# Kernel optimization log

Hardware: AMD Instinct MI355X
Metric: run time of the kernel (lower is better)

Reference implementation:

```python
import jax, jax.numpy as jnp
import numpy as np

D_MODEL = 1024
N_HEAD = 16
HEAD_DIM = D_MODEL // N_HEAD


def setup_inputs() -> dict:
    key = jax.random.key(0)
    ks = jax.random.split(key, 5)
    B, T = 2, 2048
    s = 1.0 / np.sqrt(D_MODEL)
    return {
        "x": jax.random.normal(ks[0], (B, T, D_MODEL), dtype=jnp.float32),
        "w_qkv": jax.random.normal(ks[1], (D_MODEL, 3 * D_MODEL), dtype=jnp.float32) * s,
        "b_qkv": jnp.zeros((3 * D_MODEL,), dtype=jnp.float32),
        "w_proj": jax.random.normal(ks[2], (D_MODEL, D_MODEL), dtype=jnp.float32) * s,
        "b_proj": jnp.zeros((D_MODEL,), dtype=jnp.float32),
    }


def reference(x, w_qkv, b_qkv, w_proj, b_proj):
    B, T, C = x.shape
    H, Dh = N_HEAD, HEAD_DIM
    scale = Dh ** -0.5
    qkv = x @ w_qkv + b_qkv                      # [B,T,3C]
    q, k, v = jnp.split(qkv, 3, axis=2)
    # [B,T,C] -> [B,H,T,Dh]
    q = q.reshape(B, T, H, Dh).transpose(0, 2, 1, 3)
    k = k.reshape(B, T, H, Dh).transpose(0, 2, 1, 3)
    v = v.reshape(B, T, H, Dh).transpose(0, 2, 1, 3)
    att = jnp.einsum("bhqd,bhkd->bhqk", q, k) * scale  # [B,H,T,T]
    causal = jnp.tril(jnp.ones((T, T), dtype=bool))
    att = jnp.where(causal, att, -jnp.inf)
    att = jax.nn.softmax(att, axis=-1)
    out = jnp.einsum("bhqk,bhkd->bhqd", att, v)  # [B,H,T,Dh]
    out = out.transpose(0, 2, 1, 3).reshape(B, T, C)
    return out @ w_proj + b_proj
```

## Files before the change

kernel.cpp:

```cpp
#include <hip/hip_runtime.h>
#include <hip/hip_bf16.h>

#define B_ 2
#define T_ 2048
#define C_ 1024
#define H_ 16
#define DH_ 64

typedef __attribute__((ext_vector_type(8))) short bf16x8;
typedef __attribute__((ext_vector_type(4))) float f32x4;
typedef __attribute__((ext_vector_type(4))) unsigned int u32x4;

#define DEVI static __device__ __forceinline__

DEVI unsigned short f2bf(float f) {
  unsigned int u = __float_as_uint(f);
  u = (u + 0x7fffu + ((u >> 16) & 1u)) >> 16;
  return (unsigned short)u;
}

DEVI f32x4 mfma16(bf16x8 a, bf16x8 b, f32x4 c) {
  return __builtin_amdgcn_mfma_f32_16x16x32_bf16(a, b, c, 0, 0, 0);
}

DEVI void gload_lds16(const unsigned short* g, unsigned short* l) {
  __builtin_amdgcn_global_load_lds(
      (const __attribute__((address_space(1))) unsigned int*)g,
      (__attribute__((address_space(3))) unsigned int*)l, 16, 0, 0);
}

DEVI unsigned int cvtpk_bf16(float lo, float hi) {
  unsigned int r;
  asm("v_cvt_pk_bf16_f32 %0, %1, %2" : "=v"(r) : "v"(lo), "v"(hi));
  return r;
}

DEVI int kperm(int kv) {
  return (kv & 3) | (((kv >> 3) & 1) << 2) | (((kv >> 5) & 1) << 3) |
         (((kv >> 2) & 1) << 4) | (((kv >> 4) & 1) << 5);
}

__global__ __launch_bounds__(256) void prep_kernel(
    const float* __restrict__ x, const float* __restrict__ w_qkv,
    const float* __restrict__ w_proj, unsigned short* __restrict__ xb,
    unsigned short* __restrict__ wqkvT, unsigned short* __restrict__ wprojT) {
  __shared__ float tile[32][33];
  int b = blockIdx.x, tid = threadIdx.x;
  if (b < 4096) {
    int i = b * 256 + tid;
    float4 v = reinterpret_cast<const float4*>(x)[i];
    ushort4 o;
    o.x = f2bf(v.x); o.y = f2bf(v.y); o.z = f2bf(v.z); o.w = f2bf(v.w);
    reinterpret_cast<ushort4*>(xb)[i] = o;
  } else {
    const float* in;
    unsigned short* out;
    int R, C, bb;
    if (b < 7168) { bb = b - 4096; in = w_qkv; out = wqkvT; R = 1024; C = 3072; }
    else          { bb = b - 7168; in = w_proj; out = wprojT; R = 1024; C = 1024; }
    int nbx = C >> 5;
    int c0 = (bb % nbx) * 32, r0 = (bb / nbx) * 32;
    int tx = tid & 31, ty = tid >> 5;
#pragma unroll
    for (int j = 0; j < 32; j += 8)
      tile[ty + j][tx] = in[(size_t)(r0 + ty + j) * C + c0 + tx];
    __syncthreads();
#pragma unroll
    for (int j = 0; j < 32; j += 8)
      out[(size_t)(c0 + ty + j) * R + r0 + tx] = f2bf(tile[tx][ty + j]);
  }
}

__global__ __launch_bounds__(256, 2) void gemm192_qkv(
    const unsigned short* __restrict__ A, const unsigned short* __restrict__ Bt,
    const float* __restrict__ bias,
    unsigned short* __restrict__ qbuf, unsigned short* __restrict__ kbuf,
    unsigned short* __restrict__ vtbuf) {
  __shared__ __attribute__((aligned(16))) unsigned short As[2][128 * 64];
  __shared__ __attribute__((aligned(16))) unsigned short Bs[2][192 * 64];
  const int Kd = 1024;
  int tid = threadIdx.x;
  int lane = tid & 63, w = tid >> 6;
  int wn = w;
  int lrow = lane & 15, lgrp = lane >> 4;

  int g = blockIdx.x;
  int gs = (g & 7) * 64 + (g >> 3);
  int by = gs >> 4, bx = gs & 15;
  int bm = by * 128, bn = bx * 192;
  const unsigned short* Ab = A + (size_t)bm * Kd;
  const unsigned short* Bb = Bt + (size_t)bn * Kd;

  int sL[2], scl[2];
#pragma unroll
  for (int it = 0; it < 2; ++it) {
    int c = tid + it * 256;
    int L = c >> 3, s = c & 7, v = s ^ (L & 7);
    sL[it] = L;
    scl[it] = (v >> 2) * 32 + (v & 3) * 8;
  }

  auto stgA = [&](int t, int h) {
    unsigned short* dst = As[t & 1] + h * 4096;
    int k0 = t << 6;
#pragma unroll
    for (int it = 0; it < 2; ++it)
      gload_lds16(Ab + (size_t)(h * 64 + sL[it]) * Kd + k0 + scl[it],
                  dst + (tid + it * 256) * 8);
  };
  auto stgB3 = [&](int t, int th) {
    unsigned short* dst = Bs[t & 1] + th * 4096;
    int k0 = t << 6;
#pragma unroll
    for (int it = 0; it < 2; ++it)
      gload_lds16(Bb + (size_t)(th * 64 + sL[it]) * Kd + k0 + scl[it],
                  dst + (tid + it * 256) * 8);
  };

  auto lda = [&](const unsigned short* buf, int mi, int kk) -> bf16x8 {
    int row = mi * 16 + lrow;
    int s = ((kk << 2) | lgrp) ^ (row & 7);
    return *reinterpret_cast<const bf16x8*>((const char*)buf + row * 128 + s * 16);
  };
  auto ldb = [&](const unsigned short* buf, int ni, int kk) -> bf16x8 {
    int row = wn * 48 + ni * 16 + lrow;
    int s = ((kk << 2) | lgrp) ^ (row & 7);
    return *reinterpret_cast<const bf16x8*>((const char*)buf + row * 128 + s * 16);
  };

  f32x4 acc[8][3] = {};
  bf16x8 bfr[3][2], af[2][2];

#define PHASE_TAIL                                          \
  __builtin_amdgcn_s_barrier();                             \
  asm volatile("s_waitcnt lgkmcnt(0)" ::: "memory");        \
  __builtin_amdgcn_sched_barrier(0);                        \
  __builtin_amdgcn_s_setprio(1);

#define MFMA_TRI(base)                                      \
  _Pragma("unroll") for (int ii = 0; ii < 2; ++ii)          \
  _Pragma("unroll") for (int ni = 0; ni < 3; ++ni) {        \
    acc[(base) + ii][ni] = mfma16(af[ii][0], bfr[ni][0], acc[(base) + ii][ni]); \
    acc[(base) + ii][ni] = mfma16(af[ii][1], bfr[ni][1], acc[(base) + ii][ni]); \
  }

#define PHASE_END                                           \
  __builtin_amdgcn_s_setprio(0);                            \
  __builtin_amdgcn_s_barrier();

  stgA(0, 0); stgA(0, 1);
  stgB3(0, 0); stgB3(0, 1); stgB3(0, 2);
  stgB3(1, 0); stgB3(1, 1); stgB3(1, 2);
  asm volatile("s_waitcnt vmcnt(6)" ::: "memory");
  __builtin_amdgcn_s_barrier();

#pragma unroll 1
  for (int j = 0; j < 8; ++j) {
    const bool nl = (j < 7);
    const int t1 = 2 * j + 1, t2 = 2 * j + 2, t3 = 2 * j + 3;

#pragma unroll
    for (int ni = 0; ni < 3; ++ni) { bfr[ni][0] = ldb(Bs[0], ni, 0); bfr[ni][1] = ldb(Bs[0], ni, 1); }
    af[0][0] = lda(As[0], 0, 0); af[0][1] = lda(As[0], 0, 1);
    af[1][0] = lda(As[0], 1, 0); af[1][1] = lda(As[0], 1, 1);
    stgA(t1, 0);
    PHASE_TAIL; MFMA_TRI(0); PHASE_END;

    af[0][0] = lda(As[0], 2, 0); af[0][1] = lda(As[0], 2, 1);
    af[1][0] = lda(As[0], 3, 0); af[1][1] = lda(As[0], 3, 1);
    stgA(t1, 1);
    if (nl) stgB3(t2, 0);
    PHASE_TAIL; MFMA_TRI(2); PHASE_END;

    af[0][0] = lda(As[0], 4, 0); af[0][1] = lda(As[0], 4, 1);
    af[1][0] = lda(As[0], 5, 0); af[1][1] = lda(As[0], 5, 1);
    if (nl) stgB3(t2, 1);
    PHASE_TAIL; MFMA_TRI(4); PHASE_END;

    af[0][0] = lda(As[0], 6, 0); af[0][1] = lda(As[0], 6, 1);
    af[1][0] = lda(As[0], 7, 0); af[1][1] = lda(As[0], 7, 1);
    if (nl) stgB3(t2, 2);
    PHASE_TAIL; MFMA_TRI(6);
    __builtin_amdgcn_s_setprio(0);
    if (nl) { asm volatile("s_waitcnt vmcnt(6)" ::: "memory"); }
    else    { asm volatile("s_waitcnt vmcnt(0)" ::: "memory"); }
    __builtin_amdgcn_s_barrier();

#pragma unroll
    for (int ni = 0; ni < 3; ++ni) { bfr[ni][0] = ldb(Bs[1], ni, 0); bfr[ni][1] = ldb(Bs[1], ni, 1); }
    af[0][0] = lda(As[1], 0, 0); af[0][1] = lda(As[1], 0, 1);
    af[1][0] = lda(As[1], 1, 0); af[1][1] = lda(As[1], 1, 1);
    if (nl) stgA(t2, 0);
    PHASE_TAIL; MFMA_TRI(0); PHASE_END;

    af[0][0] = lda(As[1], 2, 0); af[0][1] = lda(As[1], 2, 1);
    af[1][0] = lda(As[1], 3, 0); af[1][1] = lda(As[1], 3, 1);
    if (nl) { stgA(t2, 1); stgB3(t3, 0); }
    PHASE_TAIL; MFMA_TRI(2); PHASE_END;

    af[0][0] = lda(As[1], 4, 0); af[0][1] = lda(As[1], 4, 1);
    af[1][0] = lda(As[1], 5, 0); af[1][1] = lda(As[1], 5, 1);
    if (nl) stgB3(t3, 1);
    PHASE_TAIL; MFMA_TRI(4); PHASE_END;

    af[0][0] = lda(As[1], 6, 0); af[0][1] = lda(As[1], 6, 1);
    af[1][0] = lda(As[1], 7, 0); af[1][1] = lda(As[1], 7, 1);
    if (nl) stgB3(t3, 2);
    PHASE_TAIL; MFMA_TRI(6);
    __builtin_amdgcn_s_setprio(0);
    if (nl) { asm volatile("s_waitcnt vmcnt(6)" ::: "memory"); }
    __builtin_amdgcn_s_barrier();
  }
#undef PHASE_TAIL
#undef MFMA_TRI
#undef PHASE_END

  int c0 = bn + wn * 48;
#pragma unroll
  for (int ni = 0; ni < 3; ++ni) {
    int col = c0 + ni * 16 + lrow;
    float bv = bias[col];
    int which = col >> 10, cc = col & 1023;
    int h = cc >> 6, d = cc & 63;
#pragma unroll
    for (int mi = 0; mi < 8; ++mi) {
      int rowb = bm + mi * 16 + lgrp * 4;
      int b = rowb >> 11, tt = rowb & 2047;
      if (which == 2) {
        ushort4 pk;
        pk.x = f2bf(acc[mi][ni][0] + bv);
        pk.y = f2bf(acc[mi][ni][1] + bv);
        pk.z = f2bf(acc[mi][ni][2] + bv);
        pk.w = f2bf(acc[mi][ni][3] + bv);
        *reinterpret_cast<ushort4*>(vtbuf + ((size_t)((b * 16 + h) * 64 + d)) * T_ + tt) = pk;
      } else {
        unsigned short* dst = (which == 0) ? qbuf : kbuf;
        size_t base = ((size_t)(b * 16 + h) * T_ + tt) * DH_ + d;
#pragma unroll
        for (int r = 0; r < 4; ++r)
          dst[base + (size_t)r * DH_] = f2bf(acc[mi][ni][r] + bv);
      }
    }
  }
}

__global__ __launch_bounds__(256) void gemm_proj(
    const unsigned short* __restrict__ A, const unsigned short* __restrict__ Bt,
    const float* __restrict__ bias, float* __restrict__ outp,
    int Ndim, int Kdim) {
  __shared__ __attribute__((aligned(16))) unsigned short As[128 * 32];
  __shared__ __attribute__((aligned(16))) unsigned short Bs[128 * 32];
  int tid = threadIdx.x;
  int lane = tid & 63, w = tid >> 6;
  int wm = w >> 1, wn = w & 1;
  int lrow = lane & 15, lgrp = lane >> 4;
  int bm = blockIdx.y * 128, bn = blockIdx.x * 128;
  const unsigned short* Ab = A + (size_t)bm * Kdim;
  const unsigned short* Bb = Bt + (size_t)bn * Kdim;

  f32x4 acc[4][4] = {};
  int nk = Kdim >> 5;
  for (int kt = 0; kt < nk; ++kt) {
    int k0 = kt << 5;
    __syncthreads();
#pragma unroll
    for (int it = 0; it < 2; ++it) {
      int c = tid + it * 256;
      int row = c >> 2, kc = (c & 3) << 3;
      gload_lds16(Ab + (size_t)row * Kdim + k0 + kc, As + (size_t)c * 8);
      gload_lds16(Bb + (size_t)row * Kdim + k0 + kc, Bs + (size_t)c * 8);
    }
    __syncthreads();
    bf16x8 af[4], bfr[4];
#pragma unroll
    for (int mi = 0; mi < 4; ++mi)
      af[mi] = *reinterpret_cast<const bf16x8*>(As + (size_t)(wm * 64 + mi * 16 + lrow) * 32 + lgrp * 8);
#pragma unroll
    for (int ni = 0; ni < 4; ++ni)
      bfr[ni] = *reinterpret_cast<const bf16x8*>(Bs + (size_t)(wn * 64 + ni * 16 + lrow) * 32 + lgrp * 8);
#pragma unroll
    for (int mi = 0; mi < 4; ++mi)
#pragma unroll
      for (int ni = 0; ni < 4; ++ni)
        acc[mi][ni] = mfma16(af[mi], bfr[ni], acc[mi][ni]);
  }

  int r0 = bm + wm * 64, c0 = bn + wn * 64;
#pragma unroll
  for (int ni = 0; ni < 4; ++ni) {
    int col = c0 + ni * 16 + lrow;
    float bv = bias[col];
#pragma unroll
    for (int mi = 0; mi < 4; ++mi) {
      int rowb = r0 + mi * 16 + lgrp * 4;
#pragma unroll
      for (int r = 0; r < 4; ++r)
        outp[(size_t)(rowb + r) * Ndim + col] = acc[mi][ni][r] + bv;
    }
  }
}

__global__ __launch_bounds__(256, 4) void attn_kernel(
    const unsigned short* __restrict__ qbuf,
    const unsigned short* __restrict__ kbuf,
    const unsigned short* __restrict__ vtbuf,
    unsigned short* __restrict__ attno) {
  __shared__ __attribute__((aligned(16))) unsigned short Ks[64 * 64];
  __shared__ __attribute__((aligned(16))) unsigned short Vts[64 * 64];

  int tid = threadIdx.x;
  int lane = tid & 63, w = tid >> 6;
  int lrow = lane & 15, lgrp = lane >> 4;

  int g = blockIdx.x;
  int s = g >> 8;
  int p = (g >> 3) & 7;
  int bh = (g & 7) | (((g >> 6) & 3) << 3);
  int qb = (s == 0) ? p : (s == 1) ? (31 - p) : (s == 2) ? (8 + p) : (23 - p);
  int wq0 = qb * 64 + w * 16;
  int nkb = qb + 1;

  const unsigned short* Qb = qbuf + (size_t)bh * T_ * DH_;
  const unsigned short* Kb = kbuf + (size_t)bh * T_ * DH_;
  const unsigned short* Vb = vtbuf + (size_t)bh * DH_ * T_;

  int srow0 = tid >> 3, scol = tid & 7;
  int srow1 = srow0 + 32;
  int pk0 = kperm(srow0), pk1 = kperm(srow1);
  int soffK0 = pk0 * 128 + ((scol * 16) ^ ((pk0 & 7) << 4));
  int soffK1 = pk1 * 128 + ((scol * 16) ^ ((pk1 & 7) << 4));
  int soffV0 = srow0 * 128 + ((scol * 16) ^ ((srow0 & 7) << 4));
  int soffV1 = srow1 * 128 + ((scol * 16) ^ ((srow1 & 7) << 4));

  const float SC = 0.125f * 1.44269504f;
  int kvbase = ((lgrp & 1) << 3) | ((lgrp >> 1) << 5);
  const int koff[4] = {0, 4, 16, 20};

  bf16x8 qf[2];
#pragma unroll
  for (int ks = 0; ks < 2; ++ks)
    qf[ks] = *reinterpret_cast<const bf16x8*>(
        Qb + (size_t)(wq0 + lrow) * DH_ + ks * 32 + lgrp * 8);

  f32x4 o[4] = {};
  float l_run = 0.f;

  bf16x8 sk0, sk1, sv0, sv1;
  auto stage_load = [&](int kb) {
    sk0 = *reinterpret_cast<const bf16x8*>(Kb + (size_t)(kb * 64 + srow0) * DH_ + scol * 8);
    sk1 = *reinterpret_cast<const bf16x8*>(Kb + (size_t)(kb * 64 + srow1) * DH_ + scol * 8);
    sv0 = *reinterpret_cast<const bf16x8*>(Vb + (size_t)srow0 * T_ + kb * 64 + scol * 8);
    sv1 = *reinterpret_cast<const bf16x8*>(Vb + (size_t)srow1 * T_ + kb * 64 + scol * 8);
  };
  auto stage_write = [&]() {
    *reinterpret_cast<bf16x8*>((char*)Ks + soffK0) = sk0;
    *reinterpret_cast<bf16x8*>((char*)Ks + soffK1) = sk1;
    *reinterpret_cast<bf16x8*>((char*)Vts + soffV0) = sv0;
    *reinterpret_cast<bf16x8*>((char*)Vts + soffV1) = sv1;
  };

  stage_load(0);
#pragma unroll 1
  for (int kb = 0; kb < nkb; ++kb) {
    if (kb > 0) __syncthreads();
    stage_write();
    __syncthreads();
    if (kb + 1 < nkb) stage_load(kb + 1);

    f32x4 sreg[4] = {};
#pragma unroll
    for (int ks = 0; ks < 2; ++ks) {
      bf16x8 kf[4];
#pragma unroll
      for (int ni = 0; ni < 4; ++ni) {
        int kr = ni * 16 + lrow;
        int off = kr * 128 + (((ks * 32 + lgrp * 8) * 2) ^ ((kr & 7) << 4));
        kf[ni] = *reinterpret_cast<const bf16x8*>((const char*)Ks + off);
      }
      __builtin_amdgcn_s_setprio(1);
#pragma unroll
      for (int ni = 0; ni < 4; ++ni)
        sreg[ni] = mfma16(kf[ni], qf[ks], sreg[ni]);
      __builtin_amdgcn_s_setprio(0);
    }

    if (kb == qb) {
      int q = wq0 + lrow;
#pragma unroll
      for (int ni = 0; ni < 4; ++ni) {
        int kvb = kb * 64 + kvbase + koff[ni];
#pragma unroll
        for (int r = 0; r < 4; ++r)
          if (kvb + r > q) sreg[ni][r] = -1e30f;
      }
    }

    f32x4 e[4];
#pragma unroll
    for (int ni = 0; ni < 4; ++ni)
#pragma unroll
      for (int r = 0; r < 4; ++r)
        e[ni][r] = __builtin_amdgcn_exp2f(sreg[ni][r] * SC);

    f32x4 ts = (e[0] + e[1]) + (e[2] + e[3]);
    l_run += (ts[0] + ts[1]) + (ts[2] + ts[3]);

    unsigned int Aw[4], Bw[4];
    Aw[0] = cvtpk_bf16(e[0][0], e[0][1]); Aw[1] = cvtpk_bf16(e[0][2], e[0][3]);
    Aw[2] = cvtpk_bf16(e[1][0], e[1][1]); Aw[3] = cvtpk_bf16(e[1][2], e[1][3]);
    Bw[0] = cvtpk_bf16(e[2][0], e[2][1]); Bw[1] = cvtpk_bf16(e[2][2], e[2][3]);
    Bw[2] = cvtpk_bf16(e[3][0], e[3][1]); Bw[3] = cvtpk_bf16(e[3][2], e[3][3]);
    u32x4 p0v, p1v;
#pragma unroll
    for (int ww = 0; ww < 4; ++ww) {
      auto sw = __builtin_amdgcn_permlane32_swap(Aw[ww], Bw[ww], false, false);
      p0v[ww] = sw[0];
      p1v[ww] = sw[1];
    }
    bf16x8 pa[2];
    pa[0] = __builtin_bit_cast(bf16x8, p0v);
    pa[1] = __builtin_bit_cast(bf16x8, p1v);

#pragma unroll
    for (int ks = 0; ks < 2; ++ks) {
      bf16x8 vf[4];
#pragma unroll
      for (int di = 0; di < 4; ++di) {
        int vr = di * 16 + lrow;
        int off = vr * 128 + (((ks * 32 + lgrp * 8) * 2) ^ ((vr & 7) << 4));
        vf[di] = *reinterpret_cast<const bf16x8*>((const char*)Vts + off);
      }
      __builtin_amdgcn_s_setprio(1);
#pragma unroll
      for (int di = 0; di < 4; ++di)
        o[di] = mfma16(pa[ks], vf[di], o[di]);
      __builtin_amdgcn_s_setprio(0);
    }
  }

  float rs = l_run;
  rs += __shfl_xor(rs, 16);
  rs += __shfl_xor(rs, 32);
  float linv = 1.0f / rs;

  int b = bh >> 4, h = bh & 15;
  float lr[4];
#pragma unroll
  for (int r = 0; r < 4; ++r) lr[r] = __shfl(linv, lgrp * 4 + r);
#pragma unroll
  for (int r = 0; r < 4; ++r) {
    int q = wq0 + lgrp * 4 + r;
    size_t base = ((size_t)(b * T_ + q)) * C_ + h * 64 + lrow;
#pragma unroll
    for (int di = 0; di < 4; ++di)
      attno[base + (size_t)di * 16] = f2bf(o[di][r] * lr[r]);
  }
}

extern "C" void kernel_launch(void* const* d_in, const int* in_sizes, int n_in,
                              void* d_out, int out_size, void* d_ws, size_t ws_size,
                              hipStream_t stream) {
  const float* x      = (const float*)d_in[0];
  const float* w_qkv  = (const float*)d_in[1];
  const float* b_qkv  = (const float*)d_in[2];
  const float* w_proj = (const float*)d_in[3];
  const float* b_proj = (const float*)d_in[4];

  char* ws = (char*)d_ws;
  unsigned short* xb     = (unsigned short*)(ws + 0);
  unsigned short* wqkvT  = (unsigned short*)(ws + 8388608);
  unsigned short* wprojT = (unsigned short*)(ws + 14680064);
  unsigned short* qbuf   = (unsigned short*)(ws + 16777216);
  unsigned short* kbuf   = (unsigned short*)(ws + 25165824);
  unsigned short* vtbuf  = (unsigned short*)(ws + 33554432);
  unsigned short* attno  = (unsigned short*)(ws + 41943040);

  prep_kernel<<<8192, 256, 0, stream>>>(x, w_qkv, w_proj, xb, wqkvT, wprojT);
  gemm192_qkv<<<dim3(512), 256, 0, stream>>>(xb, wqkvT, b_qkv, qbuf, kbuf, vtbuf);
  attn_kernel<<<dim3(1024), 256, 0, stream>>>(qbuf, kbuf, vtbuf, attno);
  gemm_proj<<<dim3(8, 32), 256, 0, stream>>>(attno, wprojT, b_proj, (float*)d_out,
                                             1024, 1024);
}
```

Measured before the change: 98.20 us.

## Rewrite projection GEMM with double-buffered swizzled LDS pipeline and block remap

Replaces the simple single-buffered projection GEMM with a double-buffered, BK=64 pipeline. Global-to-LDS loads for later k-tiles are interleaved between MFMA phases, LDS rows use an XOR swizzle to avoid bank conflicts, wave priority is raised around the MFMA sections, and a 1D grid is remapped for L2 locality. The aim is to hide global load latency and LDS conflicts in the output projection. The cost is larger LDS use, hard-coded dimensions and more complex barrier/waitcnt logic.

```diff
diff --git a/kernel.cpp b/kernel.cpp
--- a/kernel.cpp
+++ b/kernel.cpp
@@ -244,58 +244,156 @@
   }
 }
 
-__global__ __launch_bounds__(256) void gemm_proj(
+__global__ __launch_bounds__(256, 2) void gemm_proj(
     const unsigned short* __restrict__ A, const unsigned short* __restrict__ Bt,
-    const float* __restrict__ bias, float* __restrict__ outp,
-    int Ndim, int Kdim) {
-  __shared__ __attribute__((aligned(16))) unsigned short As[128 * 32];
-  __shared__ __attribute__((aligned(16))) unsigned short Bs[128 * 32];
+    const float* __restrict__ bias, float* __restrict__ outp) {
+  __shared__ __attribute__((aligned(16))) unsigned short As[2][128 * 64];
+  __shared__ __attribute__((aligned(16))) unsigned short Bs[2][128 * 64];
+  const int Kd = 1024, Nd = 1024;
   int tid = threadIdx.x;
   int lane = tid & 63, w = tid >> 6;
-  int wm = w >> 1, wn = w & 1;
+  int wn = w;
   int lrow = lane & 15, lgrp = lane >> 4;
-  int bm = blockIdx.y * 128, bn = blockIdx.x * 128;
-  const unsigned short* Ab = A + (size_t)bm * Kdim;
-  const unsigned short* Bb = Bt + (size_t)bn * Kdim;
-
-  f32x4 acc[4][4] = {};
-  int nk = Kdim >> 5;
-  for (int kt = 0; kt < nk; ++kt) {
-    int k0 = kt << 5;
-    __syncthreads();
-#pragma unroll
-    for (int it = 0; it < 2; ++it) {
-      int c = tid + it * 256;
-      int row = c >> 2, kc = (c & 3) << 3;
-      gload_lds16(Ab + (size_t)row * Kdim + k0 + kc, As + (size_t)c * 8);
-      gload_lds16(Bb + (size_t)row * Kdim + k0 + kc, Bs + (size_t)c * 8);
-    }
-    __syncthreads();
-    bf16x8 af[4], bfr[4];
-#pragma unroll
-    for (int mi = 0; mi < 4; ++mi)
-      af[mi] = *reinterpret_cast<const bf16x8*>(As + (size_t)(wm * 64 + mi * 16 + lrow) * 32 + lgrp * 8);
-#pragma unroll
-    for (int ni = 0; ni < 4; ++ni)
-      bfr[ni] = *reinterpret_cast<const bf16x8*>(Bs + (size_t)(wn * 64 + ni * 16 + lrow) * 32 + lgrp * 8);
-#pragma unroll
-    for (int mi = 0; mi < 4; ++mi)
-#pragma unroll
-      for (int ni = 0; ni < 4; ++ni)
-        acc[mi][ni] = mfma16(af[mi], bfr[ni], acc[mi][ni]);
-  }
-
-  int r0 = bm + wm * 64, c0 = bn + wn * 64;
-#pragma unroll
-  for (int ni = 0; ni < 4; ++ni) {
+
+  int g = blockIdx.x;
+  int gs = (g & 7) * 32 + (g >> 3);
+  int by = gs >> 3, bx = gs & 7;
+  int bm = by * 128, bn = bx * 128;
+  const unsigned short* Ab = A + (size_t)bm * Kd;
+  const unsigned short* Bb = Bt + (size_t)bn * Kd;
+
+  int sL[2], scl[2];
+#pragma unroll
+  for (int it = 0; it < 2; ++it) {
+    int c = tid + it * 256;
+    int L = c >> 3, s = c & 7, v = s ^ (L & 7);
+    sL[it] = L;
+    scl[it] = (v >> 2) * 32 + (v & 3) * 8;
+  }
+
+  auto stgA = [&](int t, int h) {
+    unsigned short* dst = As[t & 1] + h * 4096;
+    int k0 = t << 6;
+#pragma unroll
+    for (int it = 0; it < 2; ++it)
+      gload_lds16(Ab + (size_t)(h * 64 + sL[it]) * Kd + k0 + scl[it],
+                  dst + (tid + it * 256) * 8);
+  };
+  auto stgB = [&](int t, int h) {
+    unsigned short* dst = Bs[t & 1] + h * 4096;
+    int k0 = t << 6;
+#pragma unroll
+    for (int it = 0; it < 2; ++it)
+      gload_lds16(Bb + (size_t)(h * 64 + sL[it]) * Kd + k0 + scl[it],
+                  dst + (tid + it * 256) * 8);
+  };
+
+  auto lda = [&](const unsigned short* buf, int mi, int kk) -> bf16x8 {
+    int row = mi * 16 + lrow;
+    int s = ((kk << 2) | lgrp) ^ (row & 7);
+    return *reinterpret_cast<const bf16x8*>((const char*)buf + row * 128 + s * 16);
+  };
+  auto ldb = [&](const unsigned short* buf, int ni, int kk) -> bf16x8 {
+    int row = wn * 32 + ni * 16 + lrow;
+    int s = ((kk << 2) | lgrp) ^ (row & 7);
+    return *reinterpret_cast<const bf16x8*>((const char*)buf + row * 128 + s * 16);
+  };
+
+  f32x4 acc[8][2] = {};
+  bf16x8 bfr[2][2], af[2][2];
+
+#define PHASE_TAIL                                          \
+  __builtin_amdgcn_s_barrier();                             \
+  asm volatile("s_waitcnt lgkmcnt(0)" ::: "memory");        \
+  __builtin_amdgcn_sched_barrier(0);                        \
+  __builtin_amdgcn_s_setprio(1);
+
+#define MFMA_DUO(base)                                      \
+  _Pragma("unroll") for (int ii = 0; ii < 2; ++ii)          \
+  _Pragma("unroll") for (int ni = 0; ni < 2; ++ni) {        \
+    acc[(base) + ii][ni] = mfma16(af[ii][0], bfr[ni][0], acc[(base) + ii][ni]); \
+    acc[(base) + ii][ni] = mfma16(af[ii][1], bfr[ni][1], acc[(base) + ii][ni]); \
+  }
+
+#define PHASE_END                                           \
+  __builtin_amdgcn_s_setprio(0);                            \
+  __builtin_amdgcn_s_barrier();
+
+  stgA(0, 0); stgA(0, 1); stgB(0, 0); stgB(0, 1);
+  stgB(1, 0); stgB(1, 1);
+  asm volatile("s_waitcnt vmcnt(4)" ::: "memory");
+  __builtin_amdgcn_s_barrier();
+
+#pragma unroll 1
+  for (int j = 0; j < 8; ++j) {
+    const bool nl = (j < 7);
+    const int t1 = 2 * j + 1, t2 = 2 * j + 2, t3 = 2 * j + 3;
+
+#pragma unroll
+    for (int ni = 0; ni < 2; ++ni) { bfr[ni][0] = ldb(Bs[0], ni, 0); bfr[ni][1] = ldb(Bs[0], ni, 1); }
+    af[0][0] = lda(As[0], 0, 0); af[0][1] = lda(As[0], 0, 1);
+    af[1][0] = lda(As[0], 1, 0); af[1][1] = lda(As[0], 1, 1);
+    stgA(t1, 0);
+    PHASE_TAIL; MFMA_DUO(0); PHASE_END;
+
+    af[0][0] = lda(As[0], 2, 0); af[0][1] = lda(As[0], 2, 1);
+    af[1][0] = lda(As[0], 3, 0); af[1][1] = lda(As[0], 3, 1);
+    stgA(t1, 1);
+    if (nl) stgB(t2, 0);
+    PHASE_TAIL; MFMA_DUO(2); PHASE_END;
+
+    af[0][0] = lda(As[0], 4, 0); af[0][1] = lda(As[0], 4, 1);
+    af[1][0] = lda(As[0], 5, 0); af[1][1] = lda(As[0], 5, 1);
+    if (nl) stgB(t2, 1);
+    PHASE_TAIL; MFMA_DUO(4); PHASE_END;
+
+    af[0][0] = lda(As[0], 6, 0); af[0][1] = lda(As[0], 6, 1);
+    af[1][0] = lda(As[0], 7, 0); af[1][1] = lda(As[0], 7, 1);
+    PHASE_TAIL; MFMA_DUO(6);
+    __builtin_amdgcn_s_setprio(0);
+    if (nl) { asm volatile("s_waitcnt vmcnt(4)" ::: "memory"); }
+    else    { asm volatile("s_waitcnt vmcnt(0)" ::: "memory"); }
+    __builtin_amdgcn_s_barrier();
+
+#pragma unroll
+    for (int ni = 0; ni < 2; ++ni) { bfr[ni][0] = ldb(Bs[1], ni, 0); bfr[ni][1] = ldb(Bs[1], ni, 1); }
+    af[0][0] = lda(As[1], 0, 0); af[0][1] = lda(As[1], 0, 1);
+    af[1][0] = lda(As[1], 1, 0); af[1][1] = lda(As[1], 1, 1);
+    if (nl) stgA(t2, 0);
+    PHASE_TAIL; MFMA_DUO(0); PHASE_END;
+
+    af[0][0] = lda(As[1], 2, 0); af[0][1] = lda(As[1], 2, 1);
+    af[1][0] = lda(As[1], 3, 0); af[1][1] = lda(As[1], 3, 1);
+    if (nl) { stgA(t2, 1); stgB(t3, 0); }
+    PHASE_TAIL; MFMA_DUO(2); PHASE_END;
+
+    af[0][0] = lda(As[1], 4, 0); af[0][1] = lda(As[1], 4, 1);
+    af[1][0] = lda(As[1], 5, 0); af[1][1] = lda(As[1], 5, 1);
+    if (nl) stgB(t3, 1);
+    PHASE_TAIL; MFMA_DUO(4); PHASE_END;
+
+    af[0][0] = lda(As[1], 6, 0); af[0][1] = lda(As[1], 6, 1);
+    af[1][0] = lda(As[1], 7, 0); af[1][1] = lda(As[1], 7, 1);
+    PHASE_TAIL; MFMA_DUO(6);
+    __builtin_amdgcn_s_setprio(0);
+    if (nl) { asm volatile("s_waitcnt vmcnt(4)" ::: "memory"); }
+    __builtin_amdgcn_s_barrier();
+  }
+#undef PHASE_TAIL
+#undef MFMA_DUO
+#undef PHASE_END
+
+  int c0 = bn + wn * 32;
+#pragma unroll
+  for (int ni = 0; ni < 2; ++ni) {
     int col = c0 + ni * 16 + lrow;
     float bv = bias[col];
 #pragma unroll
-    for (int mi = 0; mi < 4; ++mi) {
-      int rowb = r0 + mi * 16 + lgrp * 4;
+    for (int mi = 0; mi < 8; ++mi) {
+      int rowb = bm + mi * 16 + lgrp * 4;
 #pragma unroll
       for (int r = 0; r < 4; ++r)
-        outp[(size_t)(rowb + r) * Ndim + col] = acc[mi][ni][r] + bv;
+        outp[(size_t)(rowb + r) * Nd + col] = acc[mi][ni][r] + bv;
     }
   }
 }
@@ -478,6 +576,5 @@
   prep_kernel<<<8192, 256, 0, stream>>>(x, w_qkv, w_proj, xb, wqkvT, wprojT);
   gemm192_qkv<<<dim3(512), 256, 0, stream>>>(xb, wqkvT, b_qkv, qbuf, kbuf, vtbuf);
   attn_kernel<<<dim3(1024), 256, 0, stream>>>(qbuf, kbuf, vtbuf, attno);
-  gemm_proj<<<dim3(8, 32), 256, 0, stream>>>(attno, wprojT, b_proj, (float*)d_out,
-                                             1024, 1024);
-}
+  gemm_proj<<<dim3(256), 256, 0, stream>>>(attno, wprojT, b_proj, (float*)d_out);
+}
```

After: 91.99 us. -6.3%, faster.
